# Performance work log

Hardware: AMD Instinct MI355X
Metric: run time of the kernel (lower is better)

The kernel has to match this reference:

```python
import jax, jax.numpy as jnp
import numpy as np

N = 10000      # nodes
E = 320000     # edges
IN = 256       # in_dim == out_dim
H = 8          # heads
D = 32         # head_dim = in_dim // heads
CLAMP = 5.0
BN_EPS = 1e-5


def setup_inputs() -> dict:
    key = jax.random.key(0)
    ks = jax.random.split(key, 24)
    s = 0.05
    nrm = lambda k, shape, sc=s: (jax.random.normal(k, shape, jnp.float32) * sc)
    inp = {
        "x": nrm(ks[0], (N, IN), 1.0),
        "edge_attr": nrm(ks[1], (E, IN), 1.0),
        "log_deg": jax.random.uniform(ks[2], (N, 1), jnp.float32, 0.1, 3.0),
        "edge_index": jax.random.randint(ks[3], (2, E), 0, N, jnp.int32),
        # attention projections (stored [in, out]; x @ W + b)
        "Qw": nrm(ks[4], (IN, H * D)), "Qb": jnp.zeros((H * D,), jnp.float32),
        "Kw": nrm(ks[5], (IN, H * D)), "Kb": jnp.zeros((H * D,), jnp.float32),
        "Ew": nrm(ks[6], (IN, H * D * 2)), "Eb": jnp.zeros((H * D * 2,), jnp.float32),
        "Vw": nrm(ks[7], (IN, H * D)), "Vb": jnp.zeros((H * D,), jnp.float32),
        "Aw": nrm(ks[8], (D, H, 1)),
        "VeRow": nrm(ks[9], (D, H, D)),
        # layer params
        "deg_coef": nrm(ks[10], (1, H * D, 2)),
        "Now": nrm(ks[11], (H * D, IN)), "Nob": jnp.zeros((IN,), jnp.float32),
        "Eow": nrm(ks[12], (H * D, IN)), "Eob": jnp.zeros((IN,), jnp.float32),
        "bn1n_g": jnp.ones((IN,), jnp.float32), "bn1n_b": jnp.zeros((IN,), jnp.float32),
        "bn1e_g": jnp.ones((IN,), jnp.float32), "bn1e_b": jnp.zeros((IN,), jnp.float32),
        "f1w": nrm(ks[13], (IN, 2 * IN)), "f1b": jnp.zeros((2 * IN,), jnp.float32),
        "f2w": nrm(ks[14], (2 * IN, IN)), "f2b": jnp.zeros((IN,), jnp.float32),
        "bn2_g": jnp.ones((IN,), jnp.float32), "bn2_b": jnp.zeros((IN,), jnp.float32),
    }
    return inp


def _bn(x, g, b):
    # batch_norm with batch statistics (bn_no_runner=True => track_running_stats=False)
    mu = jnp.mean(x, axis=0)
    var = jnp.mean(jnp.square(x - mu), axis=0)  # biased, as torch BN
    return (x - mu) * jax.lax.rsqrt(var + BN_EPS) * g + b


def _attention(x, edge_attr, edge_index, Qw, Qb, Kw, Kb, Ew, Eb, Vw, Vb, Aw, VeRow):
    n = x.shape[0]
    src, dst = edge_index[0], edge_index[1]
    Qh = (x @ Qw + Qb).reshape(n, H, D)
    Kh = (x @ Kw + Kb).reshape(n, H, D)
    Vh = (x @ Vw + Vb).reshape(n, H, D)
    Ex = (edge_attr @ Ew + Eb).reshape(-1, H, 2 * D)
    score1 = Kh[src] + Qh[dst]                      # [E,H,D]
    s2 = Ex[:, :, :D] * Ex[:, :, D:]
    score2 = jnp.sign(s2) * jnp.sqrt(jnp.abs(s2))   # == sqrt(relu(s2)) - sqrt(relu(-s2))
    conn = jax.nn.relu(score1 + score2)             # [E,H,D] (attn act='relu')
    score = jnp.einsum('ehd,dhc->ehc', conn, Aw)    # [E,H,1]
    score = jnp.clip(score, -CLAMP, CLAMP)
    # segment softmax over destination nodes
    m = jax.ops.segment_max(score, dst, num_segments=n)
    e = jnp.exp(score - m[dst])
    ssum = jax.ops.segment_sum(e, dst, num_segments=n)
    attn = e / (ssum[dst] + 1e-16)                  # [E,H,1]
    msg = Vh[src] * attn
    Vo = Qh + jax.ops.segment_sum(msg, dst, num_segments=n)
    rowV = jax.ops.segment_sum(conn * attn, dst, num_segments=n)
    rowV = jnp.einsum('nhd,dhc->nhc', rowV, VeRow)
    Vo = Vo + rowV
    return Vo.reshape(n, H * D), conn.reshape(-1, H * D)


def reference(x, edge_attr, log_deg, edge_index, Qw, Qb, Kw, Kb, Ew, Eb, Vw, Vb,
              Aw, VeRow, deg_coef, Now, Nob, Eow, Eob, bn1n_g, bn1n_b,
              bn1e_g, bn1e_b, f1w, f1b, f2w, f2b, bn2_g, bn2_b):
    nh, eh = _attention(x, edge_attr, edge_index, Qw, Qb, Kw, Kb, Ew, Eb, Vw, Vb, Aw, VeRow)
    # degree scaler
    nh = nh * deg_coef[:, :, 0] + (nh * log_deg) * deg_coef[:, :, 1]
    nh = nh @ Now + Nob
    eh = eh @ Eow + Eob
    nh = x + nh
    eh = edge_attr + eh
    nh = _bn(nh, bn1n_g, bn1n_b)
    eh = _bn(eh, bn1e_g, bn1e_b)
    ffn = jax.nn.relu(nh @ f1w + f1b) @ f2w + f2b
    nh = _bn(nh + ffn, bn2_g, bn2_b)
    return nh, eh
```

## Files before the change

kernel.cpp:

```cpp
#include <hip/hip_runtime.h>

#define NN 10000
#define NE 320000

typedef float f4 __attribute__((ext_vector_type(4)));
typedef float f32x4 __attribute__((ext_vector_type(4)));
typedef short bf16x8 __attribute__((ext_vector_type(8)));

__device__ __forceinline__ unsigned short f2b(float f) {
  unsigned u = __float_as_uint(f);
  u += 0x7fff + ((u >> 16) & 1);
  return (unsigned short)(u >> 16);
}
__device__ __forceinline__ float b2f(unsigned short s) {
  return __uint_as_float(((unsigned)s) << 16);
}
__device__ __forceinline__ bf16x8 pack8(f4 a, f4 b) {
  bf16x8 r;
  r[0] = (short)f2b(a[0]); r[1] = (short)f2b(a[1]);
  r[2] = (short)f2b(a[2]); r[3] = (short)f2b(a[3]);
  r[4] = (short)f2b(b[0]); r[5] = (short)f2b(b[1]);
  r[6] = (short)f2b(b[2]); r[7] = (short)f2b(b[3]);
  return r;
}
__device__ __forceinline__ int swz(int row, int k) {
  return (row * 256 + k) ^ ((row & 7) << 3);
}

__global__ void castw_k(const float* __restrict__ in, unsigned short* __restrict__ out,
                        int K, int lg)
{
  int idx = blockIdx.x * 256 + threadIdx.x;
  if (idx >= (K << lg)) return;
  int n = idx & ((1 << lg) - 1), k = idx >> lg;
  out[(size_t)n * K + k] = f2b(in[idx]);
}

__global__ __launch_bounds__(256) void gemm_bf16_k(
    const float* __restrict__ A, const unsigned short* __restrict__ BT,
    const float* __restrict__ bias, const float* __restrict__ res,
    float* __restrict__ C, float* __restrict__ stats,
    int M, int K, int NT, int flags)
{
  __shared__ unsigned short Al[64][40];
  __shared__ unsigned short Bl[128][40];
  const int t = threadIdx.x;
  const int n0 = blockIdx.x * 128;
  const int m0 = blockIdx.y * 64;
  const int lane = t & 63, c = lane & 15, g = lane >> 4, w = t >> 6;
  f32x4 acc[8] = {};
  for (int k0 = 0; k0 < K; k0 += 32) {
    {
      int row = t >> 2, kk = (t & 3) * 8;
      f4 v0 = {0.f,0.f,0.f,0.f}, v1 = {0.f,0.f,0.f,0.f};
      if (m0 + row < M) {
        const f4* p = (const f4*)(A + (size_t)(m0 + row) * K + k0 + kk);
        v0 = p[0]; v1 = p[1];
      }
      __syncthreads();
      *(bf16x8*)&Al[row][kk] = pack8(v0, v1);
    }
    {
      int col = t >> 1, kk = (t & 1) * 16;
      const bf16x8* p = (const bf16x8*)(BT + (size_t)(n0 + col) * K + k0 + kk);
      *(bf16x8*)&Bl[col][kk] = p[0];
      *(bf16x8*)&Bl[col][kk + 8] = p[1];
    }
    __syncthreads();
    bf16x8 a = *(bf16x8*)&Al[w * 16 + c][g * 8];
#pragma unroll
    for (int nb = 0; nb < 8; nb++) {
      bf16x8 b = *(bf16x8*)&Bl[nb * 16 + c][g * 8];
      acc[nb] = __builtin_amdgcn_mfma_f32_16x16x32_bf16(a, b, acc[nb], 0, 0, 0);
    }
  }
  const int do_relu = flags & 1, do_stats = flags & 2;
#pragma unroll
  for (int nb = 0; nb < 8; nb++) {
    const int col = n0 + nb * 16 + c;
    const float bs = bias[col];
    float sn = 0.f, qn = 0.f;
#pragma unroll
    for (int r = 0; r < 4; r++) {
      int row = m0 + w * 16 + g * 4 + r;
      if (row < M) {
        float v = acc[nb][r] + bs;
        if (res) v += res[(size_t)row * NT + col];
        if (do_relu) v = fmaxf(v, 0.f);
        C[(size_t)row * NT + col] = v;
        sn += v; qn += v * v;
      }
    }
    if (do_stats) {
      sn += __shfl_xor(sn, 16); sn += __shfl_xor(sn, 32);
      qn += __shfl_xor(qn, 16); qn += __shfl_xor(qn, 32);
      if (g == 0) {
        atomicAdd(&stats[col], sn);
        atomicAdd(&stats[NT + col], qn);
      }
    }
  }
}

__global__ __launch_bounds__(256) void edge_conn_k(
    const float* __restrict__ EA, const unsigned short* __restrict__ EwT,
    const float* __restrict__ Eb, const float* __restrict__ Kh,
    const float* __restrict__ Qh, const int* __restrict__ ei,
    const float* __restrict__ Aw, float* __restrict__ conn, float* __restrict__ score)
{
  __shared__ unsigned short Abuf[16384];
  __shared__ unsigned short Bbuf[16384];
  float* Exl = (float*)Bbuf;
  const int t = threadIdx.x;
  const int e0 = blockIdx.x * 64;
  const int lane = t & 63, c = lane & 15, g = lane >> 4, w = t >> 6;
#pragma unroll
  for (int it = 0; it < 8; it++) {
    int o = t + it * 256;
    int row = o >> 5, kk = (o & 31) * 8;
    const f4* p = (const f4*)(EA + (size_t)(e0 + row) * 256 + kk);
    f4 v0 = p[0], v1 = p[1];
    *(bf16x8*)&Abuf[swz(row, kk)] = pack8(v0, v1);
  }
  const int m2 = t >> 2, dg = t & 3;
  const int e = e0 + m2;
  const int src = ei[e], dst = ei[NE + e];
  for (int h = 0; h < 8; h++) {
    __syncthreads();
#pragma unroll
    for (int it = 0; it < 8; it++) {
      int o = t + it * 256;
      int row = o >> 5, kk = (o & 31) * 8;
      *(bf16x8*)&Bbuf[swz(row, kk)] =
          *(const bf16x8*)(EwT + (size_t)(h * 64 + row) * 256 + kk);
    }
    __syncthreads();
    f32x4 acc[4] = {};
#pragma unroll
    for (int ks = 0; ks < 8; ks++) {
      bf16x8 a = *(bf16x8*)&Abuf[swz(w * 16 + c, ks * 32 + g * 8)];
#pragma unroll
      for (int cb = 0; cb < 4; cb++) {
        bf16x8 b = *(bf16x8*)&Bbuf[swz(cb * 16 + c, ks * 32 + g * 8)];
        acc[cb] = __builtin_amdgcn_mfma_f32_16x16x32_bf16(a, b, acc[cb], 0, 0, 0);
      }
    }
    __syncthreads();
#pragma unroll
    for (int cb = 0; cb < 4; cb++) {
      float eb = Eb[h * 64 + cb * 16 + c];
#pragma unroll
      for (int r = 0; r < 4; r++)
        Exl[(w * 16 + g * 4 + r) * 68 + cb * 16 + c] = acc[cb][r] + eb;
    }
    __syncthreads();
    const int cb2 = h * 32 + dg * 8;
    const float* ex = Exl + m2 * 68;
    f4 x1a = *(const f4*)(ex + dg * 8);
    f4 x1b = *(const f4*)(ex + dg * 8 + 4);
    f4 x2a = *(const f4*)(ex + 32 + dg * 8);
    f4 x2b = *(const f4*)(ex + 32 + dg * 8 + 4);
    f4 k1 = *(const f4*)(Kh + (size_t)src * 256 + cb2);
    f4 k2 = *(const f4*)(Kh + (size_t)src * 256 + cb2 + 4);
    f4 q1 = *(const f4*)(Qh + (size_t)dst * 256 + cb2);
    f4 q2 = *(const f4*)(Qh + (size_t)dst * 256 + cb2 + 4);
    f4 c1, c2;
    float part = 0.f;
#pragma unroll
    for (int j = 0; j < 4; j++) {
      float s2 = x1a[j] * x2a[j];
      float v = copysignf(sqrtf(fabsf(s2)), s2) + k1[j] + q1[j];
      v = fmaxf(v, 0.f);
      c1[j] = v;
      part += v * Aw[(dg * 8 + j) * 8 + h];
      float s2b = x1b[j] * x2b[j];
      float vb = copysignf(sqrtf(fabsf(s2b)), s2b) + k2[j] + q2[j];
      vb = fmaxf(vb, 0.f);
      c2[j] = vb;
      part += vb * Aw[(dg * 8 + 4 + j) * 8 + h];
    }
    *(f4*)(conn + (size_t)e * 256 + cb2) = c1;
    *(f4*)(conn + (size_t)e * 256 + cb2 + 4) = c2;
    part += __shfl_xor(part, 1);
    part += __shfl_xor(part, 2);
    if (dg == 0) score[(size_t)e * 8 + h] = fminf(fmaxf(part, -5.f), 5.f);
  }
}

__global__ void hist_k(const int* __restrict__ ei, int* __restrict__ cnt)
{
  int e = blockIdx.x * 256 + threadIdx.x;
  if (e < NE) atomicAdd(&cnt[ei[NE + e]], 1);
}

__global__ __launch_bounds__(256) void scan_k(const int* __restrict__ cnt, int* __restrict__ off)
{
  __shared__ int part[256];
  const int t = threadIdx.x;
  const int PER = 40;
  const int base = t * PER;
  int s = 0;
  for (int i = 0; i < PER; i++) {
    int b = base + i;
    if (b < NN) s += cnt[b];
  }
  part[t] = s;
  __syncthreads();
  for (int d = 1; d < 256; d <<= 1) {
    int v = (t >= d) ? part[t - d] : 0;
    __syncthreads();
    part[t] += v;
    __syncthreads();
  }
  int run = (t == 0) ? 0 : part[t - 1];
  for (int i = 0; i < PER; i++) {
    int b = base + i;
    if (b < NN) { off[b] = run; run += cnt[b]; }
  }
  if (t == 255) off[NN] = run;
}

__global__ void scat_k(const int* __restrict__ ei, const int* __restrict__ off,
                       int* __restrict__ cur, int* __restrict__ elist)
{
  int e = blockIdx.x * 256 + threadIdx.x;
  if (e < NE) {
    int d = ei[NE + e];
    int p = atomicAdd(&cur[d], 1);
    elist[off[d] + p] = e;
  }
}

__global__ __launch_bounds__(256) void node_agg_k(
    const int* __restrict__ off, const int* __restrict__ elist,
    const int* __restrict__ ei, const float* __restrict__ score,
    const float* __restrict__ Vh, const float* __restrict__ conn,
    const float* __restrict__ Qh, const float* __restrict__ VeRow,
    const float* __restrict__ deg_coef, const float* __restrict__ log_deg,
    float* __restrict__ nh_a)
{
  const int n = blockIdx.x, t = threadIdx.x;
  const int h = t >> 5;
  __shared__ int eL[128];
  __shared__ int srcL[128];
  __shared__ float sS[128 * 8];
  __shared__ float rA[256];
  const int start = off[n];
  const int deg = off[n + 1] - start;
  float m = -1e30f, ssum = 0.f, vo = 0.f, ro = 0.f;
  for (int c0 = 0; c0 < deg; c0 += 128) {
    const int cn = min(128, deg - c0);
    __syncthreads();
    if (t < cn) {
      int e = elist[start + c0 + t];
      eL[t] = e;
      srcL[t] = ei[e];
    }
    __syncthreads();
    for (int i = t; i < cn * 8; i += 256) sS[i] = score[(size_t)eL[i >> 3] * 8 + (i & 7)];
    __syncthreads();
    float mc = -1e30f;
    for (int i = 0; i < cn; i++) mc = fmaxf(mc, sS[i * 8 + h]);
    float nm = fmaxf(m, mc);
    float sc = __expf(m - nm);
    ssum *= sc; vo *= sc; ro *= sc;
    m = nm;
    for (int i = 0; i < cn; i++) {
      float w = __expf(sS[i * 8 + h] - m);
      ssum += w;
      vo = fmaf(w, Vh[(size_t)srcL[i] * 256 + t], vo);
      ro = fmaf(w, conn[(size_t)eL[i] * 256 + t], ro);
    }
  }
  const float inv = 1.f / (ssum + 1e-16f);
  vo *= inv;
  ro *= inv;
  __syncthreads();
  rA[t] = ro;
  __syncthreads();
  float acc = 0.f;
#pragma unroll
  for (int d = 0; d < 32; d++) acc = fmaf(rA[h * 32 + d], VeRow[d * 256 + t], acc);
  float v = Qh[(size_t)n * 256 + t] + vo + acc;
  const float ld = log_deg[n];
  v = v * (deg_coef[2 * t] + ld * deg_coef[2 * t + 1]);
  nh_a[(size_t)n * 256 + t] = v;
}

__global__ __launch_bounds__(256) void eh_gemm_k(
    const unsigned short* __restrict__ EowT, const float* __restrict__ Eob,
    const float* __restrict__ EA, float* __restrict__ eh, float* __restrict__ stb)
{
  __shared__ unsigned short Al[64][264];
  __shared__ unsigned short Bl[256][40];
  __shared__ float lsum[256], lsq[256];
  const int t = threadIdx.x;
  const int e0 = blockIdx.x * 64;
  const int lane = t & 63, c = lane & 15, g = lane >> 4, w = t >> 6;
  lsum[t] = 0.f; lsq[t] = 0.f;
#pragma unroll
  for (int it = 0; it < 8; it++) {
    int o = t + it * 256;
    int row = o >> 5, kk = (o & 31) * 8;
    const f4* p = (const f4*)(eh + (size_t)(e0 + row) * 256 + kk);
    f4 v0 = p[0], v1 = p[1];
    *(bf16x8*)&Al[row][kk] = pack8(v0, v1);
  }
  f32x4 acc[16] = {};
  for (int ks = 0; ks < 8; ks++) {
    __syncthreads();
#pragma unroll
    for (int it = 0; it < 4; it++) {
      int o = t + it * 256;
      int row = o >> 2, kk = (o & 3) * 8;
      *(bf16x8*)&Bl[row][kk] = *(const bf16x8*)(EowT + (size_t)row * 256 + ks * 32 + kk);
    }
    __syncthreads();
    bf16x8 a = *(bf16x8*)&Al[w * 16 + c][ks * 32 + g * 8];
#pragma unroll
    for (int nb = 0; nb < 16; nb++) {
      bf16x8 b = *(bf16x8*)&Bl[nb * 16 + c][g * 8];
      acc[nb] = __builtin_amdgcn_mfma_f32_16x16x32_bf16(a, b, acc[nb], 0, 0, 0);
    }
  }
#pragma unroll
  for (int nb = 0; nb < 16; nb++) {
    const int col = nb * 16 + c;
    const float eob = Eob[col];
    float sn = 0.f, qn = 0.f;
#pragma unroll
    for (int r = 0; r < 4; r++) {
      size_t row = e0 + w * 16 + g * 4 + r;
      float v = acc[nb][r] + eob + EA[row * 256 + col];
      eh[row * 256 + col] = v;
      sn += v; qn += v * v;
    }
    sn += __shfl_xor(sn, 16); sn += __shfl_xor(sn, 32);
    qn += __shfl_xor(qn, 16); qn += __shfl_xor(qn, 32);
    if (g == 0) { atomicAdd(&lsum[col], sn); atomicAdd(&lsq[col], qn); }
  }
  __syncthreads();
  float* dstb = stb + (size_t)(blockIdx.x & 63) * 512;
  atomicAdd(&dstb[t], lsum[t]);
  atomicAdd(&dstb[256 + t], lsq[t]);
}

__global__ void bn_fin_k(float* __restrict__ st, float invR)
{
  int t = threadIdx.x;
  float mean = st[t] * invR;
  float var = st[256 + t] * invR - mean * mean;
  st[t] = mean;
  st[256 + t] = rsqrtf(var + 1e-5f);
}

__global__ void bn_fin_banked_k(const float* __restrict__ banks, float* __restrict__ st,
                                float invR)
{
  int t = threadIdx.x;
  float s = 0.f, q = 0.f;
  for (int b = 0; b < 64; b++) {
    s += banks[(size_t)b * 512 + t];
    q += banks[(size_t)b * 512 + 256 + t];
  }
  float mean = s * invR;
  float var = q * invR - mean * mean;
  st[t] = mean;
  st[256 + t] = rsqrtf(var + 1e-5f);
}

__global__ void bn_apply_k(const float* __restrict__ X, float* __restrict__ Y,
                           const float* __restrict__ st, const float* __restrict__ g,
                           const float* __restrict__ b, long nvec)
{
  long i = (long)blockIdx.x * 256 + threadIdx.x;
  if (i >= nvec) return;
  int base = (int)(i & 63) * 4;
  f4 x = *(const f4*)(X + i * 4);
  f4 mn = *(const f4*)(st + base);
  f4 rs = *(const f4*)(st + 256 + base);
  f4 gg = *(const f4*)(g + base);
  f4 bb = *(const f4*)(b + base);
  f4 y;
#pragma unroll
  for (int j = 0; j < 4; j++) y[j] = (x[j] - mn[j]) * rs[j] * gg[j] + bb[j];
  *(f4*)(Y + i * 4) = y;
}

extern "C" void kernel_launch(void* const* d_in, const int* in_sizes, int n_in,
                              void* d_out, int out_size, void* d_ws, size_t ws_size,
                              hipStream_t stream)
{
  (void)in_sizes; (void)n_in; (void)out_size; (void)ws_size;
  const float* x        = (const float*)d_in[0];
  const float* edge_attr= (const float*)d_in[1];
  const float* log_deg  = (const float*)d_in[2];
  const int*   ei       = (const int*)d_in[3];
  const float* Qw = (const float*)d_in[4];  const float* Qb = (const float*)d_in[5];
  const float* Kw = (const float*)d_in[6];  const float* Kb = (const float*)d_in[7];
  const float* Ew = (const float*)d_in[8];  const float* Eb = (const float*)d_in[9];
  const float* Vw = (const float*)d_in[10]; const float* Vb = (const float*)d_in[11];
  const float* Aw = (const float*)d_in[12]; const float* VeRow = (const float*)d_in[13];
  const float* deg_coef = (const float*)d_in[14];
  const float* Now = (const float*)d_in[15]; const float* Nob = (const float*)d_in[16];
  const float* Eow = (const float*)d_in[17]; const float* Eob = (const float*)d_in[18];
  const float* bn1n_g = (const float*)d_in[19]; const float* bn1n_b = (const float*)d_in[20];
  const float* bn1e_g = (const float*)d_in[21]; const float* bn1e_b = (const float*)d_in[22];
  const float* f1w = (const float*)d_in[23]; const float* f1b = (const float*)d_in[24];
  const float* f2w = (const float*)d_in[25]; const float* f2b = (const float*)d_in[26];
  const float* bn2_g = (const float*)d_in[27]; const float* bn2_b = (const float*)d_in[28];

  float* out_nh = (float*)d_out;
  float* out_eh = out_nh + (size_t)NN * 256;

  float* ws     = (float*)d_ws;
  float* Qh     = ws;
  float* Kh     = Qh + 2560000;
  float* Vh     = Kh + 2560000;
  float* score  = Vh + 2560000;
  float* nh_a   = score + 2560000;
  float* nh2    = nh_a + 2560000;
  float* ffn1   = nh2 + 2560000;
  float* st1    = ffn1 + 5120000;
  float* st2    = st1 + 512;
  float* st3    = st2 + 512;
  float* stb    = st3 + 512;
  unsigned short* QwT = (unsigned short*)(stb + 64 * 512);
  unsigned short* KwT = QwT + 65536;
  unsigned short* VwT = KwT + 65536;
  unsigned short* NowT= VwT + 65536;
  unsigned short* EowT= NowT + 65536;
  unsigned short* EwT = EowT + 65536;
  unsigned short* f1wT= EwT + 131072;
  unsigned short* f2wT= f1wT + 131072;
  int*   cnt    = (int*)(f2wT + 131072);
  int*   off    = cnt + NN;
  int*   cur    = off + NN + 1;
  int*   elist  = cur + NN;

  hipMemsetAsync(cnt, 0, (size_t)NN * 4, stream);
  hipMemsetAsync(cur, 0, (size_t)NN * 4, stream);
  hipMemsetAsync(st1, 0, (size_t)2 * 512 * 4, stream);
  hipMemsetAsync(stb, 0, (size_t)64 * 512 * 4, stream);

  dim3 blk(256);

  castw_k<<<dim3(256), blk, 0, stream>>>(Qw, QwT, 256, 8);
  castw_k<<<dim3(256), blk, 0, stream>>>(Kw, KwT, 256, 8);
  castw_k<<<dim3(256), blk, 0, stream>>>(Vw, VwT, 256, 8);
  castw_k<<<dim3(256), blk, 0, stream>>>(Now, NowT, 256, 8);
  castw_k<<<dim3(256), blk, 0, stream>>>(Eow, EowT, 256, 8);
  castw_k<<<dim3(512), blk, 0, stream>>>(Ew, EwT, 256, 9);
  castw_k<<<dim3(512), blk, 0, stream>>>(f1w, f1wT, 256, 9);
  castw_k<<<dim3(512), blk, 0, stream>>>(f2w, f2wT, 512, 8);

  hist_k<<<dim3(NE / 256), blk, 0, stream>>>(ei, cnt);
  scan_k<<<dim3(1), blk, 0, stream>>>(cnt, off);
  scat_k<<<dim3(NE / 256), blk, 0, stream>>>(ei, off, cur, elist);

  gemm_bf16_k<<<dim3(2, 157), blk, 0, stream>>>(x, QwT, Qb, nullptr, Qh, nullptr,
                                                NN, 256, 256, 0);
  gemm_bf16_k<<<dim3(2, 157), blk, 0, stream>>>(x, KwT, Kb, nullptr, Kh, nullptr,
                                                NN, 256, 256, 0);
  gemm_bf16_k<<<dim3(2, 157), blk, 0, stream>>>(x, VwT, Vb, nullptr, Vh, nullptr,
                                                NN, 256, 256, 0);

  edge_conn_k<<<dim3(NE / 64), blk, 0, stream>>>(edge_attr, EwT, Eb, Kh, Qh, ei, Aw,
                                                 out_eh, score);

  node_agg_k<<<dim3(NN), blk, 0, stream>>>(off, elist, ei, score, Vh, out_eh,
                                           Qh, VeRow, deg_coef, log_deg, nh_a);

  eh_gemm_k<<<dim3(NE / 64), blk, 0, stream>>>(EowT, Eob, edge_attr, out_eh, stb);
  bn_fin_banked_k<<<dim3(1), blk, 0, stream>>>(stb, st3, 1.0f / NE);
  bn_apply_k<<<dim3(NE * 64 / 256), blk, 0, stream>>>(out_eh, out_eh, st3,
                                                      bn1e_g, bn1e_b, (long)NE * 64);

  gemm_bf16_k<<<dim3(2, 157), blk, 0, stream>>>(nh_a, NowT, Nob, x, out_nh, st1,
                                                NN, 256, 256, 2);
  bn_fin_k<<<dim3(1), blk, 0, stream>>>(st1, 1.0f / NN);
  bn_apply_k<<<dim3(NN * 64 / 256), blk, 0, stream>>>(out_nh, nh2, st1,
                                                      bn1n_g, bn1n_b, (long)NN * 64);
  gemm_bf16_k<<<dim3(4, 157), blk, 0, stream>>>(nh2, f1wT, f1b, nullptr, ffn1, nullptr,
                                                NN, 256, 512, 1);
  gemm_bf16_k<<<dim3(2, 157), blk, 0, stream>>>(ffn1, f2wT, f2b, nh2, out_nh, st2,
                                                NN, 512, 256, 2);
  bn_fin_k<<<dim3(1), blk, 0, stream>>>(st2, 1.0f / NN);
  bn_apply_k<<<dim3(NN * 64 / 256), blk, 0, stream>>>(out_nh, out_nh, st2,
                                                      bn2_g, bn2_b, (long)NN * 64);
}
```

Baseline: 1.045 ms.

## Fuse QKV GEMM, store conn in bf16, pre-sort src ids, parallelize softmax max

Combines the Q/K/V projections into one GEMM with N=768 and a concatenated bias. When the workspace is large enough, conn is written as bf16 into a separate buffer, which is read by node aggregation and by the edge-output GEMM. This removes the fp32 conn round trip and the re-cast in eh_gemm. It also gathers source ids into CSR order during scatter, parallelizes the per-head max with warp shuffles, precomputes the exp weights in shared memory, and unrolls the aggregation loop by four. The trade-off is lower conn precision in the aggregation path, and the swizzle function changes form.

```diff
diff --git a/kernel.cpp b/kernel.cpp
--- a/kernel.cpp
+++ b/kernel.cpp
@@ -24,7 +24,7 @@
   return r;
 }
 __device__ __forceinline__ int swz(int row, int k) {
-  return (row * 256 + k) ^ ((row & 7) << 3);
+  return (row * 256) + (k ^ ((row & 7) << 3));
 }
 
 __global__ void castw_k(const float* __restrict__ in, unsigned short* __restrict__ out,
@@ -34,6 +34,13 @@
   if (idx >= (K << lg)) return;
   int n = idx & ((1 << lg) - 1), k = idx >> lg;
   out[(size_t)n * K + k] = f2b(in[idx]);
+}
+
+__global__ void cat3_k(const float* __restrict__ a, const float* __restrict__ b,
+                       const float* __restrict__ c, float* __restrict__ o)
+{
+  int t = threadIdx.x;
+  o[t] = a[t]; o[256 + t] = b[t]; o[512 + t] = c[t];
 }
 
 __global__ __launch_bounds__(256) void gemm_bf16_k(
@@ -104,9 +111,10 @@
 
 __global__ __launch_bounds__(256) void edge_conn_k(
     const float* __restrict__ EA, const unsigned short* __restrict__ EwT,
-    const float* __restrict__ Eb, const float* __restrict__ Kh,
-    const float* __restrict__ Qh, const int* __restrict__ ei,
-    const float* __restrict__ Aw, float* __restrict__ conn, float* __restrict__ score)
+    const float* __restrict__ Eb, const float* __restrict__ QKVh,
+    const int* __restrict__ ei, const float* __restrict__ Aw,
+    float* __restrict__ connf, unsigned short* __restrict__ connb,
+    float* __restrict__ score, int CB)
 {
   __shared__ unsigned short Abuf[16384];
   __shared__ unsigned short Bbuf[16384];
@@ -160,10 +168,10 @@
     f4 x1b = *(const f4*)(ex + dg * 8 + 4);
     f4 x2a = *(const f4*)(ex + 32 + dg * 8);
     f4 x2b = *(const f4*)(ex + 32 + dg * 8 + 4);
-    f4 k1 = *(const f4*)(Kh + (size_t)src * 256 + cb2);
-    f4 k2 = *(const f4*)(Kh + (size_t)src * 256 + cb2 + 4);
-    f4 q1 = *(const f4*)(Qh + (size_t)dst * 256 + cb2);
-    f4 q2 = *(const f4*)(Qh + (size_t)dst * 256 + cb2 + 4);
+    f4 k1 = *(const f4*)(QKVh + (size_t)src * 768 + 256 + cb2);
+    f4 k2 = *(const f4*)(QKVh + (size_t)src * 768 + 256 + cb2 + 4);
+    f4 q1 = *(const f4*)(QKVh + (size_t)dst * 768 + cb2);
+    f4 q2 = *(const f4*)(QKVh + (size_t)dst * 768 + cb2 + 4);
     f4 c1, c2;
     float part = 0.f;
 #pragma unroll
@@ -179,8 +187,12 @@
       c2[j] = vb;
       part += vb * Aw[(dg * 8 + 4 + j) * 8 + h];
     }
-    *(f4*)(conn + (size_t)e * 256 + cb2) = c1;
-    *(f4*)(conn + (size_t)e * 256 + cb2 + 4) = c2;
+    if (CB) {
+      *(bf16x8*)(connb + (size_t)e * 256 + cb2) = pack8(c1, c2);
+    } else {
+      *(f4*)(connf + (size_t)e * 256 + cb2) = c1;
+      *(f4*)(connf + (size_t)e * 256 + cb2 + 4) = c2;
+    }
     part += __shfl_xor(part, 1);
     part += __shfl_xor(part, 2);
     if (dg == 0) score[(size_t)e * 8 + h] = fminf(fmaxf(part, -5.f), 5.f);
@@ -221,29 +233,33 @@
 }
 
 __global__ void scat_k(const int* __restrict__ ei, const int* __restrict__ off,
-                       int* __restrict__ cur, int* __restrict__ elist)
+                       int* __restrict__ cur, int* __restrict__ elist,
+                       int* __restrict__ src_s)
 {
   int e = blockIdx.x * 256 + threadIdx.x;
   if (e < NE) {
-    int d = ei[NE + e];
+    int s = ei[e], d = ei[NE + e];
     int p = atomicAdd(&cur[d], 1);
-    elist[off[d] + p] = e;
+    int j = off[d] + p;
+    elist[j] = e;
+    src_s[j] = s;
   }
 }
 
 __global__ __launch_bounds__(256) void node_agg_k(
     const int* __restrict__ off, const int* __restrict__ elist,
-    const int* __restrict__ ei, const float* __restrict__ score,
-    const float* __restrict__ Vh, const float* __restrict__ conn,
-    const float* __restrict__ Qh, const float* __restrict__ VeRow,
-    const float* __restrict__ deg_coef, const float* __restrict__ log_deg,
-    float* __restrict__ nh_a)
+    const int* __restrict__ src_s, const float* __restrict__ score,
+    const float* __restrict__ QKVh, const float* __restrict__ connf,
+    const unsigned short* __restrict__ connb, int CB,
+    const float* __restrict__ VeRow, const float* __restrict__ deg_coef,
+    const float* __restrict__ log_deg, float* __restrict__ nh_a)
 {
   const int n = blockIdx.x, t = threadIdx.x;
   const int h = t >> 5;
   __shared__ int eL[128];
   __shared__ int srcL[128];
-  __shared__ float sS[128 * 8];
+  __shared__ float sS[1024];
+  __shared__ float mS[8];
   __shared__ float rA[256];
   const int start = off[n];
   const int deg = off[n + 1] - start;
@@ -252,24 +268,73 @@
     const int cn = min(128, deg - c0);
     __syncthreads();
     if (t < cn) {
-      int e = elist[start + c0 + t];
-      eL[t] = e;
-      srcL[t] = ei[e];
+      int jj = start + c0 + t;
+      eL[t] = elist[jj];
+      srcL[t] = src_s[jj];
     }
     __syncthreads();
     for (int i = t; i < cn * 8; i += 256) sS[i] = score[(size_t)eL[i >> 3] * 8 + (i & 7)];
     __syncthreads();
     float mc = -1e30f;
-    for (int i = 0; i < cn; i++) mc = fmaxf(mc, sS[i * 8 + h]);
+    for (int i = (t & 31); i < cn; i += 32) mc = fmaxf(mc, sS[i * 8 + h]);
+    mc = fmaxf(mc, __shfl_xor(mc, 1));
+    mc = fmaxf(mc, __shfl_xor(mc, 2));
+    mc = fmaxf(mc, __shfl_xor(mc, 4));
+    mc = fmaxf(mc, __shfl_xor(mc, 8));
+    mc = fmaxf(mc, __shfl_xor(mc, 16));
     float nm = fmaxf(m, mc);
+    if ((t & 31) == 0) mS[h] = nm;
+    __syncthreads();
+    for (int i = t; i < cn * 8; i += 256) sS[i] = __expf(sS[i] - mS[i & 7]);
+    __syncthreads();
     float sc = __expf(m - nm);
     ssum *= sc; vo *= sc; ro *= sc;
     m = nm;
-    for (int i = 0; i < cn; i++) {
-      float w = __expf(sS[i * 8 + h] - m);
-      ssum += w;
-      vo = fmaf(w, Vh[(size_t)srcL[i] * 256 + t], vo);
-      ro = fmaf(w, conn[(size_t)eL[i] * 256 + t], ro);
+    int i = 0;
+    if (CB) {
+      for (; i + 4 <= cn; i += 4) {
+        float w0 = sS[(i + 0) * 8 + h], w1 = sS[(i + 1) * 8 + h];
+        float w2 = sS[(i + 2) * 8 + h], w3 = sS[(i + 3) * 8 + h];
+        int s0 = srcL[i], s1 = srcL[i + 1], s2 = srcL[i + 2], s3 = srcL[i + 3];
+        int f0 = eL[i], f1 = eL[i + 1], f2 = eL[i + 2], f3 = eL[i + 3];
+        ssum += w0 + w1 + w2 + w3;
+        vo = fmaf(w0, QKVh[(size_t)s0 * 768 + 512 + t], vo);
+        vo = fmaf(w1, QKVh[(size_t)s1 * 768 + 512 + t], vo);
+        vo = fmaf(w2, QKVh[(size_t)s2 * 768 + 512 + t], vo);
+        vo = fmaf(w3, QKVh[(size_t)s3 * 768 + 512 + t], vo);
+        ro = fmaf(w0, b2f(connb[(size_t)f0 * 256 + t]), ro);
+        ro = fmaf(w1, b2f(connb[(size_t)f1 * 256 + t]), ro);
+        ro = fmaf(w2, b2f(connb[(size_t)f2 * 256 + t]), ro);
+        ro = fmaf(w3, b2f(connb[(size_t)f3 * 256 + t]), ro);
+      }
+      for (; i < cn; i++) {
+        float w0 = sS[i * 8 + h];
+        ssum += w0;
+        vo = fmaf(w0, QKVh[(size_t)srcL[i] * 768 + 512 + t], vo);
+        ro = fmaf(w0, b2f(connb[(size_t)eL[i] * 256 + t]), ro);
+      }
+    } else {
+      for (; i + 4 <= cn; i += 4) {
+        float w0 = sS[(i + 0) * 8 + h], w1 = sS[(i + 1) * 8 + h];
+        float w2 = sS[(i + 2) * 8 + h], w3 = sS[(i + 3) * 8 + h];
+        int s0 = srcL[i], s1 = srcL[i + 1], s2 = srcL[i + 2], s3 = srcL[i + 3];
+        int f0 = eL[i], f1 = eL[i + 1], f2 = eL[i + 2], f3 = eL[i + 3];
+        ssum += w0 + w1 + w2 + w3;
+        vo = fmaf(w0, QKVh[(size_t)s0 * 768 + 512 + t], vo);
+        vo = fmaf(w1, QKVh[(size_t)s1 * 768 + 512 + t], vo);
+        vo = fmaf(w2, QKVh[(size_t)s2 * 768 + 512 + t], vo);
+        vo = fmaf(w3, QKVh[(size_t)s3 * 768 + 512 + t], vo);
+        ro = fmaf(w0, connf[(size_t)f0 * 256 + t], ro);
+        ro = fmaf(w1, connf[(size_t)f1 * 256 + t], ro);
+        ro = fmaf(w2, connf[(size_t)f2 * 256 + t], ro);
+        ro = fmaf(w3, connf[(size_t)f3 * 256 + t], ro);
+      }
+      for (; i < cn; i++) {
+        float w0 = sS[i * 8 + h];
+        ssum += w0;
+        vo = fmaf(w0, QKVh[(size_t)srcL[i] * 768 + 512 + t], vo);
+        ro = fmaf(w0, connf[(size_t)eL[i] * 256 + t], ro);
+      }
     }
   }
   const float inv = 1.f / (ssum + 1e-16f);
@@ -281,7 +346,7 @@
   float acc = 0.f;
 #pragma unroll
   for (int d = 0; d < 32; d++) acc = fmaf(rA[h * 32 + d], VeRow[d * 256 + t], acc);
-  float v = Qh[(size_t)n * 256 + t] + vo + acc;
+  float v = QKVh[(size_t)n * 768 + t] + vo + acc;
   const float ld = log_deg[n];
   v = v * (deg_coef[2 * t] + ld * deg_coef[2 * t + 1]);
   nh_a[(size_t)n * 256 + t] = v;
@@ -289,7 +354,8 @@
 
 __global__ __launch_bounds__(256) void eh_gemm_k(
     const unsigned short* __restrict__ EowT, const float* __restrict__ Eob,
-    const float* __restrict__ EA, float* __restrict__ eh, float* __restrict__ stb)
+    const float* __restrict__ EA, const unsigned short* __restrict__ connb, int CB,
+    float* __restrict__ eh, float* __restrict__ stb)
 {
   __shared__ unsigned short Al[64][264];
   __shared__ unsigned short Bl[256][40];
@@ -302,9 +368,13 @@
   for (int it = 0; it < 8; it++) {
     int o = t + it * 256;
     int row = o >> 5, kk = (o & 31) * 8;
-    const f4* p = (const f4*)(eh + (size_t)(e0 + row) * 256 + kk);
-    f4 v0 = p[0], v1 = p[1];
-    *(bf16x8*)&Al[row][kk] = pack8(v0, v1);
+    if (CB) {
+      *(bf16x8*)&Al[row][kk] = *(const bf16x8*)(connb + (size_t)(e0 + row) * 256 + kk);
+    } else {
+      const f4* p = (const f4*)(eh + (size_t)(e0 + row) * 256 + kk);
+      f4 v0 = p[0], v1 = p[1];
+      *(bf16x8*)&Al[row][kk] = pack8(v0, v1);
+    }
   }
   f32x4 acc[16] = {};
   for (int ks = 0; ks < 8; ks++) {
@@ -391,7 +461,7 @@
                               void* d_out, int out_size, void* d_ws, size_t ws_size,
                               hipStream_t stream)
 {
-  (void)in_sizes; (void)n_in; (void)out_size; (void)ws_size;
+  (void)in_sizes; (void)n_in; (void)out_size;
   const float* x        = (const float*)d_in[0];
   const float* edge_attr= (const float*)d_in[1];
   const float* log_deg  = (const float*)d_in[2];
@@ -414,10 +484,8 @@
   float* out_eh = out_nh + (size_t)NN * 256;
 
   float* ws     = (float*)d_ws;
-  float* Qh     = ws;
-  float* Kh     = Qh + 2560000;
-  float* Vh     = Kh + 2560000;
-  float* score  = Vh + 2560000;
+  float* QKVh   = ws;
+  float* score  = QKVh + (size_t)NN * 768;
   float* nh_a   = score + 2560000;
   float* nh2    = nh_a + 2560000;
   float* ffn1   = nh2 + 2560000;
@@ -425,7 +493,8 @@
   float* st2    = st1 + 512;
   float* st3    = st2 + 512;
   float* stb    = st3 + 512;
-  unsigned short* QwT = (unsigned short*)(stb + 64 * 512);
+  float* biasQKV= stb + 64 * 512;
+  unsigned short* QwT = (unsigned short*)(biasQKV + 768);
   unsigned short* KwT = QwT + 65536;
   unsigned short* VwT = KwT + 65536;
   unsigned short* NowT= VwT + 65536;
@@ -437,6 +506,10 @@
   int*   off    = cnt + NN;
   int*   cur    = off + NN + 1;
   int*   elist  = cur + NN;
+  int*   src_s  = elist + NE;
+  unsigned short* connb = (unsigned short*)(src_s + NE);
+  size_t need = (size_t)((char*)(connb + (size_t)NE * 256) - (char*)d_ws);
+  const int CB = (ws_size >= need) ? 1 : 0;
 
   hipMemsetAsync(cnt, 0, (size_t)NN * 4, stream);
   hipMemsetAsync(cur, 0, (size_t)NN * 4, stream);
@@ -453,25 +526,24 @@
   castw_k<<<dim3(512), blk, 0, stream>>>(Ew, EwT, 256, 9);
   castw_k<<<dim3(512), blk, 0, stream>>>(f1w, f1wT, 256, 9);
   castw_k<<<dim3(512), blk, 0, stream>>>(f2w, f2wT, 512, 8);
+  cat3_k<<<dim3(1), blk, 0, stream>>>(Qb, Kb, Vb, biasQKV);
 
   hist_k<<<dim3(NE / 256), blk, 0, stream>>>(ei, cnt);
   scan_k<<<dim3(1), blk, 0, stream>>>(cnt, off);
-  scat_k<<<dim3(NE / 256), blk, 0, stream>>>(ei, off, cur, elist);
-
-  gemm_bf16_k<<<dim3(2, 157), blk, 0, stream>>>(x, QwT, Qb, nullptr, Qh, nullptr,
-                                                NN, 256, 256, 0);
-  gemm_bf16_k<<<dim3(2, 157), blk, 0, stream>>>(x, KwT, Kb, nullptr, Kh, nullptr,
-                                                NN, 256, 256, 0);
-  gemm_bf16_k<<<dim3(2, 157), blk, 0, stream>>>(x, VwT, Vb, nullptr, Vh, nullptr,
-                                                NN, 256, 256, 0);
-
-  edge_conn_k<<<dim3(NE / 64), blk, 0, stream>>>(edge_attr, EwT, Eb, Kh, Qh, ei, Aw,
-                                                 out_eh, score);
-
-  node_agg_k<<<dim3(NN), blk, 0, stream>>>(off, elist, ei, score, Vh, out_eh,
-                                           Qh, VeRow, deg_coef, log_deg, nh_a);
-
-  eh_gemm_k<<<dim3(NE / 64), blk, 0, stream>>>(EowT, Eob, edge_attr, out_eh, stb);
+  scat_k<<<dim3(NE / 256), blk, 0, stream>>>(ei, off, cur, elist, src_s);
+
+  gemm_bf16_k<<<dim3(6, 157), blk, 0, stream>>>(x, QwT, biasQKV, nullptr, QKVh, nullptr,
+                                                NN, 256, 768, 0);
+
+  edge_conn_k<<<dim3(NE / 64), blk, 0, stream>>>(edge_attr, EwT, Eb, QKVh, ei, Aw,
+                                                 out_eh, connb, score, CB);
+
+  node_agg_k<<<dim3(NN), blk, 0, stream>>>(off, elist, src_s, score, QKVh,
+                                           out_eh, connb, CB,
+                                           VeRow, deg_coef, log_deg, nh_a);
+
+  eh_gemm_k<<<dim3(NE / 64), blk, 0, stream>>>(EowT, Eob, edge_attr, connb, CB,
+                                               out_eh, stb);
   bn_fin_banked_k<<<dim3(1), blk, 0, stream>>>(stb, st3, 1.0f / NE);
   bn_apply_k<<<dim3(NE * 64 / 256), blk, 0, stream>>>(out_eh, out_eh, st3,
                                                       bn1e_g, bn1e_b, (long)NE * 64);
```

New measurement: 1.020 ms. -2.4%, faster.
